# Optimization experiments

Measured on AMD Instinct MI355X. Metric: run time of the kernel, lower is better.

## Reference

```python
import jax, jax.numpy as jnp
import numpy as np

EPS = 1e-8      # degenerate-triangle / ray-hit epsilon
CHUNK = 1024    # points processed per map step to bound peak memory


def _counts(pts, v1, e1, e2, h, f, valid):
    """Moller-Trumbore ray-triangle test with fixed ray dir d=(0,0,1).
    pts: [B,C,3]; triangle data: [F,3] / [F]. Returns [B,C] hit counts."""
    s = pts[:, :, None, :] - v1[None, None, :, :]          # [B,C,F,3]
    u = f * jnp.einsum('bcfk,fk->bcf', s, h)               # barycentric u
    q = jnp.cross(s, e1[None, None, :, :])                 # [B,C,F,3]
    v = f * q[..., 2]                                      # dot(d,q) = q_z since d=(0,0,1)
    t = f * jnp.einsum('bcfk,fk->bcf', q, e2)              # ray parameter
    hit = (valid[None, None, :] & (u >= 0) & (u <= 1) & (v >= 0)
           & (u + v <= 1) & (t > EPS))
    return hit.astype(pts.dtype).sum(-1)                   # [B,C]


def setup_inputs() -> dict:
    key = jax.random.key(0)
    k1, k2, k3, k4 = jax.random.split(key, 4)
    points = jax.random.normal(k1, (4, 16384, 3), dtype=jnp.float32)
    verts_1 = jax.random.normal(k2, (2048, 3), dtype=jnp.float32)
    verts_2 = jax.random.normal(k3, (2048, 3), dtype=jnp.float32)
    verts_3 = jax.random.normal(k4, (2048, 3), dtype=jnp.float32)
    return {"points": points, "verts_1": verts_1, "verts_2": verts_2, "verts_3": verts_3}


def reference(points, verts_1, verts_2, verts_3):
    B, N, _ = points.shape
    e1 = verts_2 - verts_1                                  # [F,3]
    e2 = verts_3 - verts_1                                  # [F,3]
    # h = cross(d, e2) with d=(0,0,1) -> (-e2_y, e2_x, 0)
    h = jnp.stack([-e2[:, 1], e2[:, 0], jnp.zeros_like(e2[:, 0])], axis=-1)
    a = jnp.einsum('fk,fk->f', e1, h)                       # determinant
    valid = jnp.abs(a) > EPS
    f = jnp.where(valid, 1.0 / jnp.where(valid, a, 1.0), 0.0)
    nc = N // CHUNK
    pts = points.reshape(B, nc, CHUNK, 3).transpose(1, 0, 2, 3)  # [nc,B,C,3]
    counts = jax.lax.map(
        lambda p: _counts(p, verts_1, e1, e2, h, f, valid), pts)  # [nc,B,C]
    return counts.transpose(1, 0, 2).reshape(B, N)
```

## Files before the change

kernel.cpp:

```cpp
#include <hip/hip_runtime.h>

#define MT_EPS 1e-8f

__global__ __launch_bounds__(256) void mt_precompute(
    const float* __restrict__ v1, const float* __restrict__ v2,
    const float* __restrict__ v3, float4* __restrict__ coef, int F)
{
    int f = blockIdx.x * 256 + threadIdx.x;
    if (f >= F) return;
    float v1x = v1[3*f+0], v1y = v1[3*f+1], v1z = v1[3*f+2];
    float v2x = v2[3*f+0], v2y = v2[3*f+1], v2z = v2[3*f+2];
    float v3x = v3[3*f+0], v3y = v3[3*f+1], v3z = v3[3*f+2];
    float e1x = v2x - v1x, e1y = v2y - v1y, e1z = v2z - v1z;
    float e2x = v3x - v1x, e2y = v3y - v1y, e2z = v3z - v1z;
    float hx = -e2y, hy = e2x;
    float a = e1x * hx + e1y * hy;
    float fi = (fabsf(a) > MT_EPS) ? (1.0f / a) : 0.0f;
    float cux = fi * hx, cuy = fi * hy;
    float cu0 = -(v1x * cux + v1y * cuy);
    float cvx = fi * e1y, cvy = -fi * e1x;
    float cv0 = -(v1x * cvx + v1y * cvy);
    float nx = e1y * e2z - e1z * e2y;
    float ny = e1z * e2x - e1x * e2z;
    float nz = e1x * e2y - e1y * e2x;
    float ctx = fi * nx, cty = fi * ny, ctz = fi * nz;
    float ct0 = -(v1x * ctx + v1y * cty + v1z * ctz);
    coef[3*f+0] = make_float4(cux, cuy, cu0, cvx);
    coef[3*f+1] = make_float4(cvy, cv0, ctx, cty);
    coef[3*f+2] = make_float4(ctz, ct0, 0.0f, 0.0f);
}

__global__ __launch_bounds__(256) void mt_count4(
    const float4* __restrict__ coef, const float* __restrict__ pts,
    float* __restrict__ out, int npts, int F, int tchunk)
{
    int tid = blockIdx.x * 256 + threadIdx.x;
    int p0 = tid * 4;
    if (p0 >= npts) return;
    const float4* pv = (const float4*)(pts + (size_t)p0 * 3);
    float4 a = pv[0], b = pv[1], c = pv[2];
    float px0 = a.x, py0 = a.y, pz0 = a.z;
    float px1 = a.w, py1 = b.x, pz1 = b.y;
    float px2 = b.z, py2 = b.w, pz2 = c.x;
    float px3 = c.y, py3 = c.z, pz3 = c.w;

    int fbase = blockIdx.y * tchunk;
    int fend  = fbase + tchunk;
    if (fend > F) fend = F;

    float cnt0 = 0.0f, cnt1 = 0.0f, cnt2 = 0.0f, cnt3 = 0.0f;
    #pragma unroll 2
    for (int f = fbase; f < fend; ++f) {
        float4 c0 = coef[3*f+0];
        float4 c1 = coef[3*f+1];
        float4 c2 = coef[3*f+2];

        {
            float u = fmaf(c0.x, px0, fmaf(c0.y, py0, c0.z));
            float v = fmaf(c0.w, px0, fmaf(c1.x, py0, c1.y));
            float t = fmaf(c1.z, px0, fmaf(c1.w, py0, fmaf(c2.x, pz0, c2.y)));
            float w = u + v;
            bool hit = (fminf(u, v) >= 0.0f) & (w <= 1.0f) & (t > MT_EPS);
            cnt0 += hit ? 1.0f : 0.0f;
        }
        {
            float u = fmaf(c0.x, px1, fmaf(c0.y, py1, c0.z));
            float v = fmaf(c0.w, px1, fmaf(c1.x, py1, c1.y));
            float t = fmaf(c1.z, px1, fmaf(c1.w, py1, fmaf(c2.x, pz1, c2.y)));
            float w = u + v;
            bool hit = (fminf(u, v) >= 0.0f) & (w <= 1.0f) & (t > MT_EPS);
            cnt1 += hit ? 1.0f : 0.0f;
        }
        {
            float u = fmaf(c0.x, px2, fmaf(c0.y, py2, c0.z));
            float v = fmaf(c0.w, px2, fmaf(c1.x, py2, c1.y));
            float t = fmaf(c1.z, px2, fmaf(c1.w, py2, fmaf(c2.x, pz2, c2.y)));
            float w = u + v;
            bool hit = (fminf(u, v) >= 0.0f) & (w <= 1.0f) & (t > MT_EPS);
            cnt2 += hit ? 1.0f : 0.0f;
        }
        {
            float u = fmaf(c0.x, px3, fmaf(c0.y, py3, c0.z));
            float v = fmaf(c0.w, px3, fmaf(c1.x, py3, c1.y));
            float t = fmaf(c1.z, px3, fmaf(c1.w, py3, fmaf(c2.x, pz3, c2.y)));
            float w = u + v;
            bool hit = (fminf(u, v) >= 0.0f) & (w <= 1.0f) & (t > MT_EPS);
            cnt3 += hit ? 1.0f : 0.0f;
        }
    }
    atomicAdd(&out[p0+0], cnt0);
    atomicAdd(&out[p0+1], cnt1);
    atomicAdd(&out[p0+2], cnt2);
    atomicAdd(&out[p0+3], cnt3);
}

extern "C" void kernel_launch(void* const* d_in, const int* in_sizes, int n_in,
                              void* d_out, int out_size, void* d_ws, size_t ws_size,
                              hipStream_t stream) {
    const float* pts = (const float*)d_in[0];
    const float* v1  = (const float*)d_in[1];
    const float* v2  = (const float*)d_in[2];
    const float* v3  = (const float*)d_in[3];
    float* out = (float*)d_out;
    int npts = in_sizes[0] / 3;
    int F    = in_sizes[1] / 3;

    float4* coef = (float4*)d_ws;

    hipMemsetAsync(d_out, 0, (size_t)out_size * sizeof(float), stream);

    mt_precompute<<<dim3((F + 255) / 256), dim3(256), 0, stream>>>(v1, v2, v3, coef, F);

    const int tsplit = 16;
    int tchunk = (F + tsplit - 1) / tsplit;
    int nthreads = (npts + 3) / 4;
    dim3 grid((nthreads + 255) / 256, tsplit);
    mt_count4<<<grid, dim3(256), 0, stream>>>(coef, pts, out, npts, F, tchunk);
}
```

Measured before the change: 65.59 us.

## Fold hit test into a single min-compare using precomputed w and shifted t

Result: faster. 61.20 us (-6.7%).

```diff
diff --git a/kernel.cpp b/kernel.cpp
--- a/kernel.cpp
+++ b/kernel.cpp
@@ -20,14 +20,17 @@
     float cu0 = -(v1x * cux + v1y * cuy);
     float cvx = fi * e1y, cvy = -fi * e1x;
     float cv0 = -(v1x * cvx + v1y * cvy);
+    float cwx = -(cux + cvx), cwy = -(cuy + cvy);
+    float cw0 = 1.0f - cu0 - cv0;
     float nx = e1y * e2z - e1z * e2y;
     float ny = e1z * e2x - e1x * e2z;
     float nz = e1x * e2y - e1y * e2x;
     float ctx = fi * nx, cty = fi * ny, ctz = fi * nz;
-    float ct0 = -(v1x * ctx + v1y * cty + v1z * ctz);
-    coef[3*f+0] = make_float4(cux, cuy, cu0, cvx);
-    coef[3*f+1] = make_float4(cvy, cv0, ctx, cty);
-    coef[3*f+2] = make_float4(ctz, ct0, 0.0f, 0.0f);
+    float ct0 = -(v1x * ctx + v1y * cty + v1z * ctz) - MT_EPS;
+    coef[4*f+0] = make_float4(cux, cuy, cu0, cvx);
+    coef[4*f+1] = make_float4(cvy, cv0, cwx, cwy);
+    coef[4*f+2] = make_float4(cw0, ctx, cty, ctz);
+    coef[4*f+3] = make_float4(ct0, 0.0f, 0.0f, 0.0f);
 }
 
 __global__ __launch_bounds__(256) void mt_count4(
@@ -48,50 +51,51 @@
     int fend  = fbase + tchunk;
     if (fend > F) fend = F;
 
-    float cnt0 = 0.0f, cnt1 = 0.0f, cnt2 = 0.0f, cnt3 = 0.0f;
-    #pragma unroll 2
+    int cnt0 = 0, cnt1 = 0, cnt2 = 0, cnt3 = 0;
+    #pragma unroll 4
     for (int f = fbase; f < fend; ++f) {
-        float4 c0 = coef[3*f+0];
-        float4 c1 = coef[3*f+1];
-        float4 c2 = coef[3*f+2];
+        float4 c0 = coef[4*f+0];
+        float4 c1 = coef[4*f+1];
+        float4 c2 = coef[4*f+2];
+        float ct0 = coef[4*f+3].x;
 
         {
             float u = fmaf(c0.x, px0, fmaf(c0.y, py0, c0.z));
             float v = fmaf(c0.w, px0, fmaf(c1.x, py0, c1.y));
-            float t = fmaf(c1.z, px0, fmaf(c1.w, py0, fmaf(c2.x, pz0, c2.y)));
-            float w = u + v;
-            bool hit = (fminf(u, v) >= 0.0f) & (w <= 1.0f) & (t > MT_EPS);
-            cnt0 += hit ? 1.0f : 0.0f;
+            float w = fmaf(c1.z, px0, fmaf(c1.w, py0, c2.x));
+            float t = fmaf(c2.y, px0, fmaf(c2.z, py0, fmaf(c2.w, pz0, ct0)));
+            float m = fminf(fminf(fminf(u, v), w), t);
+            cnt0 += (m >= 0.0f) ? 1 : 0;
         }
         {
             float u = fmaf(c0.x, px1, fmaf(c0.y, py1, c0.z));
             float v = fmaf(c0.w, px1, fmaf(c1.x, py1, c1.y));
-            float t = fmaf(c1.z, px1, fmaf(c1.w, py1, fmaf(c2.x, pz1, c2.y)));
-            float w = u + v;
-            bool hit = (fminf(u, v) >= 0.0f) & (w <= 1.0f) & (t > MT_EPS);
-            cnt1 += hit ? 1.0f : 0.0f;
+            float w = fmaf(c1.z, px1, fmaf(c1.w, py1, c2.x));
+            float t = fmaf(c2.y, px1, fmaf(c2.z, py1, fmaf(c2.w, pz1, ct0)));
+            float m = fminf(fminf(fminf(u, v), w), t);
+            cnt1 += (m >= 0.0f) ? 1 : 0;
         }
         {
             float u = fmaf(c0.x, px2, fmaf(c0.y, py2, c0.z));
             float v = fmaf(c0.w, px2, fmaf(c1.x, py2, c1.y));
-            float t = fmaf(c1.z, px2, fmaf(c1.w, py2, fmaf(c2.x, pz2, c2.y)));
-            float w = u + v;
-            bool hit = (fminf(u, v) >= 0.0f) & (w <= 1.0f) & (t > MT_EPS);
-            cnt2 += hit ? 1.0f : 0.0f;
+            float w = fmaf(c1.z, px2, fmaf(c1.w, py2, c2.x));
+            float t = fmaf(c2.y, px2, fmaf(c2.z, py2, fmaf(c2.w, pz2, ct0)));
+            float m = fminf(fminf(fminf(u, v), w), t);
+            cnt2 += (m >= 0.0f) ? 1 : 0;
         }
         {
             float u = fmaf(c0.x, px3, fmaf(c0.y, py3, c0.z));
             float v = fmaf(c0.w, px3, fmaf(c1.x, py3, c1.y));
-            float t = fmaf(c1.z, px3, fmaf(c1.w, py3, fmaf(c2.x, pz3, c2.y)));
-            float w = u + v;
-            bool hit = (fminf(u, v) >= 0.0f) & (w <= 1.0f) & (t > MT_EPS);
-            cnt3 += hit ? 1.0f : 0.0f;
+            float w = fmaf(c1.z, px3, fmaf(c1.w, py3, c2.x));
+            float t = fmaf(c2.y, px3, fmaf(c2.z, py3, fmaf(c2.w, pz3, ct0)));
+            float m = fminf(fminf(fminf(u, v), w), t);
+            cnt3 += (m >= 0.0f) ? 1 : 0;
         }
     }
-    atomicAdd(&out[p0+0], cnt0);
-    atomicAdd(&out[p0+1], cnt1);
-    atomicAdd(&out[p0+2], cnt2);
-    atomicAdd(&out[p0+3], cnt3);
+    atomicAdd(&out[p0+0], (float)cnt0);
+    atomicAdd(&out[p0+1], (float)cnt1);
+    atomicAdd(&out[p0+2], (float)cnt2);
+    atomicAdd(&out[p0+3], (float)cnt3);
 }
 
 extern "C" void kernel_launch(void* const* d_in, const int* in_sizes, int n_in,
@@ -111,7 +115,7 @@
 
     mt_precompute<<<dim3((F + 255) / 256), dim3(256), 0, stream>>>(v1, v2, v3, coef, F);
 
-    const int tsplit = 16;
+    const int tsplit = 32;
     int tchunk = (F + tsplit - 1) / tsplit;
     int nthreads = (npts + 3) / 4;
     dim3 grid((nthreads + 255) / 256, tsplit);
```
